# Performance work log

Hardware: AMD Instinct MI355X
Metric: run time of the kernel (lower is better)

Reference implementation:

```python
import jax, jax.numpy as jnp
import numpy as np

N = 50000      # nodes
E = 600000     # edges (before self loops)
F_IN = 128     # num_features
HID = 64       # num_hidden (per-head out channels of conv1)
HEADS = 8
NCLS = 16      # num_classes
NC = 16        # n_components (k_ricci feature dim)
NCP = 16       # n_components_p (e_poinc feature dim)


def _glorot(key, shape):
    lim = float(np.sqrt(6.0 / (shape[0] + shape[1])))
    return jax.random.uniform(key, shape, jnp.float32, -lim, lim)


def setup_inputs() -> dict:
    key = jax.random.key(0)
    ks = jax.random.split(key, 16)
    H1 = HEADS * HID  # 512
    return {
        "x": jax.random.normal(ks[0], (N, F_IN), jnp.float32),
        "edge_index": jax.random.randint(ks[1], (2, E), 0, N, jnp.int32),
        "alpha": jnp.ones((), jnp.float32),  # alpha_hp scalar
        "k_ricci": jax.random.normal(ks[2], (E + N, NC), jnp.float32),
        "e_poinc": jax.random.normal(ks[3], (N, NCP), jnp.float32),
        # conv1 params
        "W_src1": _glorot(ks[4], (F_IN, H1)),
        "h1_w1": _glorot(ks[5], (NC, HID)),
        "h1_w2": _glorot(ks[6], (HID, HID)),
        "h1_b2": jnp.zeros((HID,), jnp.float32),
        "p1_w1": _glorot(ks[7], (NCP, H1)),
        "p1_w2": _glorot(ks[8], (H1, H1)),
        "p1_b2": jnp.zeros((H1,), jnp.float32),
        "bias1": jnp.zeros((H1,), jnp.float32),
        # conv2 params (heads=1, concat=False)
        "W_src2": _glorot(ks[9], (H1, NCLS)),
        "h2_w1": _glorot(ks[10], (NC, NCLS)),
        "h2_w2": _glorot(ks[11], (NCLS, NCLS)),
        "h2_b2": jnp.zeros((NCLS,), jnp.float32),
        "p2_w1": _glorot(ks[12], (NCP, NCLS)),
        "p2_w2": _glorot(ks[13], (NCLS, NCLS)),
        "p2_b2": jnp.zeros((NCLS,), jnp.float32),
        "bias2": jnp.zeros((NCLS,), jnp.float32),
    }


def _segment_softmax(logits, seg, n):
    # PyG-style softmax over variable-sized segments, per channel.
    m = jax.ops.segment_max(logits, seg, num_segments=n)
    e = jnp.exp(logits - m[seg])
    s = jax.ops.segment_sum(e, seg, num_segments=n)
    return e / (s[seg] + 1e-16)


def _gat_layer(x, src, dst, k_ricci, e_poinc, alpha_hp,
               W_src, hw1, hw2, hb2, pw1, pw2, pb2, bias, H, C, concat):
    n = x.shape[0]
    xh = (x @ W_src).reshape(n, H, C)                                   # [N,H,C]
    # hmpnn MLP on per-edge Ricci features, then segment-softmax over SOURCE node
    edge_w = jax.nn.leaky_relu(k_ricci @ hw1, 0.2) @ hw2 + hb2          # [E',C]
    a = _segment_softmax(edge_w, src, n)                                # [E',C]
    msg = a[:, None, :] * xh[src]                                       # [E',H,C]
    agg = jax.ops.segment_sum(msg, dst, num_segments=n)                 # [N,H,C]
    out = agg.reshape(n, H * C) if concat else agg.mean(axis=1)
    out = out + bias
    # ham MLP on per-node Poincare features (+ extra leaky_relu, slope 0.01)
    p = jax.nn.leaky_relu(jax.nn.leaky_relu(e_poinc @ pw1, 0.2) @ pw2 + pb2, 0.01)
    return out + alpha_hp * p


def reference(x, edge_index, alpha, k_ricci, e_poinc,
              W_src1, h1_w1, h1_w2, h1_b2, p1_w1, p1_w2, p1_b2, bias1,
              W_src2, h2_w1, h2_w2, h2_b2, p2_w1, p2_w2, p2_b2, bias2):
    n = x.shape[0]
    loops = jnp.arange(n, dtype=edge_index.dtype)
    src = jnp.concatenate([edge_index[0], loops])   # add_self_loops
    dst = jnp.concatenate([edge_index[1], loops])
    h = _gat_layer(x, src, dst, k_ricci, e_poinc, alpha,
                   W_src1, h1_w1, h1_w2, h1_b2, p1_w1, p1_w2, p1_b2, bias1,
                   HEADS, HID, True)
    h = jax.nn.relu(h)
    o = _gat_layer(h, src, dst, k_ricci, e_poinc, alpha,
                   W_src2, h2_w1, h2_w2, h2_b2, p2_w1, p2_w2, p2_b2, bias2,
                   1, NCLS, False)
    return jax.nn.log_softmax(o, axis=1)
```

## Files before the change

kernel.cpp:

```cpp
#include <hip/hip_runtime.h>
#include <math.h>

#define N_NODES 50000
#define M_PAD   50048
#define N_EDGES 600000
#define E_TOT   650000
#define F_IN    128
#define HID     64
#define HEADS   8
#define H1      512
#define NCLS    16
#define NC      16
#define NCP     16
#define NBLK    ((N_NODES + 255) / 256)

typedef unsigned short u16;
typedef unsigned char  u8;
typedef __attribute__((ext_vector_type(8))) short short8;
typedef __attribute__((ext_vector_type(4))) float f32x4;
typedef __attribute__((ext_vector_type(2))) float f32x2;

__device__ __forceinline__ float bf2f(u16 h) {
    return __uint_as_float(((unsigned)h) << 16);
}
__device__ __forceinline__ u16 f2bf(float f) {
    unsigned u = __float_as_uint(f);
    u += 0x7fffu + ((u >> 16) & 1u);
    return (u16)(u >> 16);
}
__device__ __forceinline__ int edge_src(const int* __restrict__ ei, int e) {
    return (e < N_EDGES) ? ei[e] : (e - N_EDGES);
}
__device__ __forceinline__ int edge_dst(const int* __restrict__ ei, int e) {
    return (e < N_EDGES) ? ei[N_EDGES + e] : (e - N_EDGES);
}

__device__ __forceinline__ void gload16(const void* g, void* l) {
    __builtin_amdgcn_global_load_lds(
        (const __attribute__((address_space(1))) unsigned int*)g,
        (__attribute__((address_space(3))) unsigned int*)l, 16, 0, 0);
}

__global__ __launch_bounds__(256) void count_k(const int* __restrict__ ei,
                                               int* __restrict__ src_cnt, int* __restrict__ dst_cnt) {
    int e = blockIdx.x * 256 + threadIdx.x;
    if (e >= E_TOT) return;
    atomicAdd(&src_cnt[edge_src(ei, e)], 1);
    atomicAdd(&dst_cnt[edge_dst(ei, e)], 1);
}

__global__ __launch_bounds__(256) void scanA_k(const int* __restrict__ src_cnt,
                                               const int* __restrict__ dst_cnt,
                                               int* __restrict__ partials) {
    int pass = blockIdx.x >= NBLK;
    int b = blockIdx.x - pass * NBLK;
    const int* cnt = pass ? dst_cnt : src_cnt;
    int idx = b * 256 + threadIdx.x;
    int v = (idx < N_NODES) ? cnt[idx] : 0;
    __shared__ int red[4];
    #pragma unroll
    for (int off = 32; off; off >>= 1) v += __shfl_down(v, off, 64);
    if ((threadIdx.x & 63) == 0) red[threadIdx.x >> 6] = v;
    __syncthreads();
    if (threadIdx.x == 0) partials[blockIdx.x] = red[0] + red[1] + red[2] + red[3];
}

__global__ __launch_bounds__(512) void scanB_k(int* __restrict__ partials) {
    __shared__ int lds[512];
    int t = threadIdx.x;
    int seg = t >> 8, i = t & 255;
    int v = (i < NBLK) ? partials[seg * NBLK + i] : 0;
    lds[t] = v;
    __syncthreads();
    for (int d = 1; d < 256; d <<= 1) {
        int x = (i >= d) ? lds[seg * 256 + i - d] : 0;
        __syncthreads();
        lds[t] += x;
        __syncthreads();
    }
    if (i < NBLK) partials[seg * NBLK + i] = lds[t] - v;
}

__global__ __launch_bounds__(256) void scanC_k(const int* __restrict__ src_cnt,
                                               const int* __restrict__ dst_cnt,
                                               const int* __restrict__ partials,
                                               int* __restrict__ src_off, int* __restrict__ dst_off) {
    int pass = blockIdx.x >= NBLK;
    int b = blockIdx.x - pass * NBLK;
    const int* cnt = pass ? dst_cnt : src_cnt;
    int* off = pass ? dst_off : src_off;
    int base = partials[blockIdx.x];
    __shared__ int lds[256];
    int t = threadIdx.x;
    int idx = b * 256 + t;
    int v = (idx < N_NODES) ? cnt[idx] : 0;
    lds[t] = v;
    __syncthreads();
    for (int d = 1; d < 256; d <<= 1) {
        int x = (t >= d) ? lds[t - d] : 0;
        __syncthreads();
        lds[t] += x;
        __syncthreads();
    }
    if (idx < N_NODES) off[idx] = base + lds[t] - v;
    if (b == 0 && t == 0) off[N_NODES] = E_TOT;
}

__global__ __launch_bounds__(256) void fill_csr_k(const int* __restrict__ ei,
                                                  const int* __restrict__ src_off, const int* __restrict__ dst_off,
                                                  int* __restrict__ src_cur, int* __restrict__ dst_cur,
                                                  int* __restrict__ src_list, int* __restrict__ rkd,
                                                  int* __restrict__ dsrc) {
    int e = blockIdx.x * 256 + threadIdx.x;
    if (e >= E_TOT) return;
    int s = edge_src(ei, e), d = edge_dst(ei, e);
    int pd = atomicAdd(&dst_cur[d], 1);
    int rd = dst_off[d] + pd;
    rkd[e] = rd;
    dsrc[rd] = s;
    int ps = atomicAdd(&src_cur[s], 1);
    src_list[src_off[s] + ps] = rd;
}

__global__ __launch_bounds__(256) void conv_a_k(const float* __restrict__ A, u16* __restrict__ Ap,
                                                int M, int Mp, int K) {
    int i = blockIdx.x * 256 + threadIdx.x;
    int total = (K >> 3) * Mp;
    if (i >= total) return;
    int r = i % Mp;
    int kb = i / Mp;
    u16* o = Ap + (size_t)i * 8;
    u16 tmp[8];
    if (r < M) {
        const float* a = A + (size_t)r * K + kb * 8;
        #pragma unroll
        for (int j = 0; j < 8; ++j) tmp[j] = f2bf(a[j]);
    } else {
        #pragma unroll
        for (int j = 0; j < 8; ++j) tmp[j] = 0;
    }
    *(ushort4*)o = *(ushort4*)tmp;
    *(ushort4*)(o + 4) = *(ushort4*)(tmp + 4);
}

__global__ __launch_bounds__(256) void conv_b_k(const float* __restrict__ B, u16* __restrict__ Bp,
                                                int K, int N) {
    int i = blockIdx.x * 256 + threadIdx.x;
    int total = (K >> 3) * N;
    if (i >= total) return;
    int n = i % N;
    int kb = i / N;
    u16 tmp[8];
    #pragma unroll
    for (int j = 0; j < 8; ++j) tmp[j] = f2bf(B[(size_t)(kb * 8 + j) * N + n]);
    u16* o = Bp + (size_t)i * 8;
    *(ushort4*)o = *(ushort4*)tmp;
    *(ushort4*)(o + 4) = *(ushort4*)(tmp + 4);
}

__device__ __forceinline__ void wfrag_one(const float* W, u16* o, int i, int K, int N) {
    int j = i & 7, lane = (i >> 3) & 63, rest = i >> 9;
    int nt = rest % (N / 16), ks = rest / (N / 16);
    int lm = lane & 15, quad = lane >> 4;
    int k = ks * 32 + quad * 8 + j, n = nt * 16 + lm;
    o[i] = (k < K) ? f2bf(W[(size_t)k * N + n]) : (u16)0;
}
__global__ __launch_bounds__(256) void wfrag_all_k(
    const float* __restrict__ h1w1, const float* __restrict__ h1w2,
    const float* __restrict__ h2w1, const float* __restrict__ h2w2,
    u16* __restrict__ w1f, u16* __restrict__ w2f,
    u16* __restrict__ w3f, u16* __restrict__ w4f) {
    int i = blockIdx.x * 256 + threadIdx.x;
    if (i < 2048)      wfrag_one(h1w1, w1f, i, 16, 64);
    else if (i < 6144) wfrag_one(h1w2, w2f, i - 2048, 64, 64);
    else if (i < 6656) wfrag_one(h2w1, w3f, i - 6144, 16, 16);
    else if (i < 7168) wfrag_one(h2w2, w4f, i - 6656, 16, 16);
}

template<int EPI>
__global__ __launch_bounds__(256) void mfma_gemm_k(
    const u16* __restrict__ Ap, const u16* __restrict__ Bp, u16* __restrict__ C,
    int M, int Mp, int Nn, int K,
    const float* __restrict__ bias, const u16* __restrict__ extra,
    const float* __restrict__ bias2, const float* __restrict__ alpha_p)
{
    __shared__ __align__(16) u16 LB[4][4096];
    const int t = threadIdx.x;
    const int wave = t >> 6, lane = t & 63;
    const int wm = (wave >> 1) * 64, wn = (wave & 1) * 64;
    const int lm = lane & 15, quad = lane >> 4;

    const int nwg = (int)(gridDim.y << 2);
    const int bid = (int)(blockIdx.y * 4 + blockIdx.x);
    const int qq = nwg >> 3, rr8 = nwg & 7;
    const int xcd = bid & 7, idx = bid >> 3;
    const int wg = (xcd < rr8 ? xcd * (qq + 1) : rr8 * (qq + 1) + (xcd - rr8) * qq) + idx;
    const int bn = (wg & 3) * 128;
    const int bm = (wg >> 2) * 128;

    const char* Ab = (const char*)Ap;
    const char* Bb = (const char*)Bp;

    f32x4 acc[4][4] = {};
    const int NT = K >> 5;

    auto stage = [&](int buf, int ts) {
        const int kb0 = ts * 4;
        #pragma unroll
        for (int h = 0; h < 2; ++h) {
            const int ob = h * 4096 + wave * 1024;
            const int kb = kb0 + (ob >> 11);
            const int rem = (ob & 1024) + lane * 16;
            gload16(Ab + ((size_t)kb * Mp + bm) * 16 + rem, (char*)LB[buf] + ob);
            gload16(Bb + ((size_t)kb * Nn + bn) * 16 + rem, (char*)LB[2 + buf] + ob);
        }
    };
    auto compute = [&](int cb) {
        const u16* As = LB[cb];
        const u16* Bs = LB[2 + cb];
        short8 af[4], bfv[4];
        #pragma unroll
        for (int mi = 0; mi < 4; ++mi)
            af[mi] = *(const short8*)(As + quad * 1024 + (wm + mi * 16 + lm) * 8);
        #pragma unroll
        for (int nj = 0; nj < 4; ++nj)
            bfv[nj] = *(const short8*)(Bs + quad * 1024 + (wn + nj * 16 + lm) * 8);
        #pragma unroll
        for (int mi = 0; mi < 4; ++mi)
            #pragma unroll
            for (int nj = 0; nj < 4; ++nj)
                acc[mi][nj] = __builtin_amdgcn_mfma_f32_16x16x32_bf16(af[mi], bfv[nj], acc[mi][nj], 0, 0, 0);
    };

    stage(0, 0);
    __syncthreads();
    int cur = 0;
    for (int ts = 0; ts < NT - 1; ++ts) {
        stage(cur ^ 1, ts + 1);
        compute(cur);
        __syncthreads();
        cur ^= 1;
    }
    compute(cur);
    __syncthreads();

    float* Tf = (float*)LB;
    const int lrow = t & 63, chunk = t >> 6;
    const int col0 = chunk * 32;
    const float alpha = (EPI == 0) ? 0.f : *alpha_p;
    #pragma unroll
    for (int pass = 0; pass < 2; ++pass) {
        if ((wave >> 1) == pass) {
            #pragma unroll
            for (int mi = 0; mi < 4; ++mi)
                #pragma unroll
                for (int r4 = 0; r4 < 4; ++r4) {
                    const int lr = mi * 16 + quad * 4 + r4;
                    const int sw = (lr & 7) << 2;
                    #pragma unroll
                    for (int nj = 0; nj < 4; ++nj)
                        Tf[lr * 128 + ((wn + nj * 16 + lm) ^ sw)] = acc[mi][nj][r4];
                }
        }
        __syncthreads();
        const int rr = bm + pass * 64 + lrow;
        if (rr < M) {
            const int sw = (lrow & 7) << 2;
            float v[32];
            #pragma unroll
            for (int j4 = 0; j4 < 8; ++j4) {
                float4 f = *(const float4*)&Tf[lrow * 128 + ((col0 + j4 * 4) ^ sw)];
                v[j4 * 4] = f.x; v[j4 * 4 + 1] = f.y; v[j4 * 4 + 2] = f.z; v[j4 * 4 + 3] = f.w;
            }
            const int gc0 = bn + col0;
            u16 pk[32];
            if (EPI == 0) {
                #pragma unroll
                for (int j = 0; j < 32; ++j) pk[j] = f2bf(v[j]);
            } else {
                const u16* ex = extra + (size_t)rr * Nn + gc0;
                #pragma unroll
                for (int g = 0; g < 4; ++g) {
                    short8 e8 = *(const short8*)(ex + g * 8);
                    #pragma unroll
                    for (int j = 0; j < 8; ++j) {
                        const int cj = g * 8 + j;
                        float vv = v[cj] + bias[gc0 + cj];
                        vv = vv > 0.f ? vv : 0.01f * vv;
                        float o = bf2f((u16)e8[j]) + bias2[gc0 + cj] + alpha * vv;
                        o = fmaxf(o, 0.f);
                        pk[cj] = f2bf(o);
                    }
                }
            }
            #pragma unroll
            for (int g = 0; g < 4; ++g)
                *(short8*)(C + (size_t)rr * Nn + gc0 + g * 8) = *(const short8*)&pk[g * 8];
        }
        __syncthreads();
    }
}

__global__ __launch_bounds__(256) void gemm_t1_k(
    const float* __restrict__ ep, const float* __restrict__ W, u16* __restrict__ t1p)
{
    __shared__ float Bs[16][64];
    const int bm = blockIdx.y * 64, bn = blockIdx.x * 64;
    const int t = threadIdx.x;
    const int tx = t & 15, ty = t >> 4;
    *(float4*)&Bs[t >> 4][(t & 15) * 4] = *(const float4*)&W[(size_t)(t >> 4) * H1 + bn + (t & 15) * 4];
    __syncthreads();
    const int r0 = bm + ty * 4;
    const int c0 = bn + tx * 4;
    for (int i = 0; i < 4; ++i) {
        int r = r0 + i;
        if (r >= N_NODES) continue;
        float av[16];
        #pragma unroll
        for (int j4 = 0; j4 < 16; j4 += 4) {
            float4 v = *(const float4*)(ep + (size_t)r * NCP + j4);
            av[j4] = v.x; av[j4 + 1] = v.y; av[j4 + 2] = v.z; av[j4 + 3] = v.w;
        }
        u16 pk[4];
        #pragma unroll
        for (int q = 0; q < 4; ++q) {
            float s = 0.f;
            #pragma unroll
            for (int k = 0; k < 16; ++k) s = fmaf(av[k], Bs[k][tx * 4 + q], s);
            s = s > 0.f ? s : 0.2f * s;
            pk[q] = f2bf(s);
        }
        u16* o = t1p + ((size_t)(c0 >> 3) * M_PAD + r) * 8 + (c0 & 7);
        *(ushort4*)o = *(ushort4*)pk;
    }
}

__global__ __launch_bounds__(256) void gemm_n16_k(
    const u16* __restrict__ A, const float* __restrict__ B, float* __restrict__ C,
    int M, int K)
{
    __shared__ float As[16][64];
    __shared__ float Bs[64][16];
    const int row0 = blockIdx.x * 16;
    const int t = threadIdx.x;
    const int r = t >> 4, c = t & 15;
    const int ar = t >> 4, ak4 = (t & 15) * 4;
    const int bk = t >> 2, bc4 = (t & 3) * 4;
    float acc = 0.f;
    for (int k0 = 0; k0 < K; k0 += 64) {
        float4 av = make_float4(0.f, 0.f, 0.f, 0.f);
        if (row0 + ar < M) {
            ushort4 h4 = *(const ushort4*)(A + (size_t)(row0 + ar) * K + k0 + ak4);
            av = make_float4(bf2f(h4.x), bf2f(h4.y), bf2f(h4.z), bf2f(h4.w));
        }
        *(float4*)&As[ar][ak4] = av;
        *(float4*)&Bs[bk][bc4] = *(const float4*)(B + (size_t)(k0 + bk) * 16 + bc4);
        __syncthreads();
        #pragma unroll
        for (int kk = 0; kk < 64; ++kk)
            acc = fmaf(As[r][kk], Bs[kk][c], acc);
        __syncthreads();
    }
    if (row0 + r < M) C[(size_t)(row0 + r) * 16 + c] = acc;
}

#define TSTR 72
__global__ __launch_bounds__(256) void edge_mlps_k(
    const float* __restrict__ kr, const int* __restrict__ rkd,
    const u16* __restrict__ w1f, const u16* __restrict__ w2f, const float* __restrict__ b2a,
    const u16* __restrict__ w3f, const u16* __restrict__ w4f, const float* __restrict__ b2b,
    u16* __restrict__ ebd, u16* __restrict__ ebd2)
{
    __shared__ __align__(16) u16 T[4][16 * TSTR];
    const int t = threadIdx.x, wv = t >> 6, lane = t & 63;
    const int lm = lane & 15, quad = lane >> 4;
    const int tile = blockIdx.x * 4 + wv;
    const int e0 = tile * 16;
    if (e0 >= E_TOT) return;
    u16* Tw = T[wv];

    short8 W1[4], W2[2][4];
    #pragma unroll
    for (int nt = 0; nt < 4; ++nt) W1[nt] = *(const short8*)(w1f + ((size_t)nt * 64 + lane) * 8);
    #pragma unroll
    for (int ks = 0; ks < 2; ++ks)
        #pragma unroll
        for (int nt = 0; nt < 4; ++nt)
            W2[ks][nt] = *(const short8*)(w2f + (((size_t)ks * 4 + nt) * 64 + lane) * 8);
    short8 W3 = *(const short8*)(w3f + (size_t)lane * 8);
    short8 W4 = *(const short8*)(w4f + (size_t)lane * 8);
    float b2av[4];
    #pragma unroll
    for (int nt = 0; nt < 4; ++nt) b2av[nt] = b2a[nt * 16 + lm];
    float b2bv = b2b[lm];

    short8 af = {};
    if (quad < 2) {
        const float* kp = kr + (size_t)(e0 + lm) * NC + quad * 8;
        float4 v0 = *(const float4*)kp;
        float4 v1 = *(const float4*)(kp + 4);
        u16 tmp[8] = {f2bf(v0.x), f2bf(v0.y), f2bf(v0.z), f2bf(v0.w),
                      f2bf(v1.x), f2bf(v1.y), f2bf(v1.z), f2bf(v1.w)};
        af = *(const short8*)tmp;
    }

    f32x4 a1[4] = {};
    #pragma unroll
    for (int nt = 0; nt < 4; ++nt)
        a1[nt] = __builtin_amdgcn_mfma_f32_16x16x32_bf16(af, W1[nt], a1[nt], 0, 0, 0);
    #pragma unroll
    for (int nt = 0; nt < 4; ++nt)
        #pragma unroll
        for (int r = 0; r < 4; ++r) {
            float v = a1[nt][r];
            v = v > 0.f ? v : 0.2f * v;
            Tw[(quad * 4 + r) * TSTR + nt * 16 + lm] = f2bf(v);
        }
    __builtin_amdgcn_s_waitcnt(0);

    short8 a2[2];
    #pragma unroll
    for (int ks = 0; ks < 2; ++ks)
        a2[ks] = *(const short8*)&Tw[lm * TSTR + ks * 32 + quad * 8];
    f32x4 c2[4] = {};
    #pragma unroll
    for (int nt = 0; nt < 4; ++nt)
        #pragma unroll
        for (int ks = 0; ks < 2; ++ks)
            c2[nt] = __builtin_amdgcn_mfma_f32_16x16x32_bf16(a2[ks], W2[ks][nt], c2[nt], 0, 0, 0);
    #pragma unroll
    for (int nt = 0; nt < 4; ++nt)
        #pragma unroll
        for (int r = 0; r < 4; ++r)
            Tw[(quad * 4 + r) * TSTR + nt * 16 + lm] = f2bf(__expf(c2[nt][r] + b2av[nt]));
    __builtin_amdgcn_s_waitcnt(0);
    #pragma unroll
    for (int p = 0; p < 2; ++p) {
        int c = p * 64 + lane;
        int row = c >> 3, off = (c & 7) * 8;
        int rd = rkd[e0 + row];
        short8 v = *(const short8*)&Tw[row * TSTR + off];
        *(short8*)(ebd + (size_t)rd * HID + off) = v;
    }

    f32x4 b1 = __builtin_amdgcn_mfma_f32_16x16x32_bf16(af, W3, (f32x4){}, 0, 0, 0);
    __builtin_amdgcn_s_waitcnt(0);
    #pragma unroll
    for (int r = 0; r < 4; ++r) {
        float v = b1[r];
        v = v > 0.f ? v : 0.2f * v;
        Tw[(quad * 4 + r) * TSTR + lm] = f2bf(v);
    }
    __builtin_amdgcn_s_waitcnt(0);
    short8 a3 = *(const short8*)&Tw[lm * TSTR + quad * 8];
    f32x4 c3 = __builtin_amdgcn_mfma_f32_16x16x32_bf16(a3, W4, (f32x4){}, 0, 0, 0);
    #pragma unroll
    for (int r = 0; r < 4; ++r)
        Tw[(quad * 4 + r) * TSTR + lm] = f2bf(__expf(c3[r] + b2bv));
    __builtin_amdgcn_s_waitcnt(0);
    if (lane < 32) {
        int row = lane >> 1, off = (lane & 1) * 8;
        int rd = rkd[e0 + row];
        short8 v = *(const short8*)&Tw[row * TSTR + off];
        *(short8*)(ebd2 + (size_t)rd * NCLS + off) = v;
    }
}

__global__ __launch_bounds__(256) void s1inv_k(
    const u16* __restrict__ ebd, const int* __restrict__ src_off, const int* __restrict__ src_list,
    u16* __restrict__ xb)
{
    __shared__ float sinv[4][64];
    int gid = blockIdx.x * 256 + threadIdx.x;
    int wid = gid >> 6, lane = gid & 63, wv = threadIdx.x >> 6;
    if (wid >= N_NODES) return;
    int o0 = src_off[wid], o1 = src_off[wid + 1];
    float s0 = 0.f, s1 = 0.f, s2 = 0.f, s3 = 0.f;
    int i = o0;
    for (; i + 3 < o1; i += 4) {
        int l0 = src_list[i], l1 = src_list[i + 1], l2 = src_list[i + 2], l3 = src_list[i + 3];
        s0 += bf2f(ebd[(size_t)l0 * HID + lane]);
        s1 += bf2f(ebd[(size_t)l1 * HID + lane]);
        s2 += bf2f(ebd[(size_t)l2 * HID + lane]);
        s3 += bf2f(ebd[(size_t)l3 * HID + lane]);
    }
    for (; i < o1; ++i) {
        int sl = src_list[i];
        s0 += bf2f(ebd[(size_t)sl * HID + lane]);
    }
    sinv[wv][lane] = 1.f / (((s0 + s1) + (s2 + s3)) + 1e-16f);
    __builtin_amdgcn_s_waitcnt(0);

    const u16* xr = xb + (size_t)wid * H1 + lane * 8;
    short8 x8 = *(const short8*)xr;
    float y[8];
    #pragma unroll
    for (int j = 0; j < 8; ++j)
        y[j] = bf2f((u16)x8[j]) * sinv[wv][(lane * 8 + j) & 63];
    int p0 = 0, p1 = 0;
    p0 = __builtin_amdgcn_cvt_pk_fp8_f32(y[0], y[1], p0, false);
    p0 = __builtin_amdgcn_cvt_pk_fp8_f32(y[2], y[3], p0, true);
    p1 = __builtin_amdgcn_cvt_pk_fp8_f32(y[4], y[5], p1, false);
    p1 = __builtin_amdgcn_cvt_pk_fp8_f32(y[6], y[7], p1, true);
    uint2 pk; pk.x = (unsigned)p0; pk.y = (unsigned)p1;
    *(uint2*)((u8*)xb + (size_t)wid * (H1 * 2) + lane * 8) = pk;
}

__global__ __launch_bounds__(256) void msg1_k(
    const u16* __restrict__ ebd, const u8* __restrict__ xq,
    const int* __restrict__ dsrc, const int* __restrict__ dst_off,
    u16* __restrict__ aggb)
{
    int gid = blockIdx.x * 256 + threadIdx.x;
    int wid = gid >> 6, lane = gid & 63;
    if (wid >= N_NODES) return;
    int o0 = dst_off[wid], o1 = dst_off[wid + 1];
    const int a_off = (lane & 7) * 8;
    float acc[8] = {};
    int i = o0;
    for (; i + 3 < o1; i += 4) {
        int s0 = __builtin_nontemporal_load(dsrc + i);
        int s1 = __builtin_nontemporal_load(dsrc + i + 1);
        int s2 = __builtin_nontemporal_load(dsrc + i + 2);
        int s3 = __builtin_nontemporal_load(dsrc + i + 3);
        short8 a0 = __builtin_nontemporal_load((const short8*)(ebd + (size_t)i * HID + a_off));
        short8 a1 = __builtin_nontemporal_load((const short8*)(ebd + (size_t)(i + 1) * HID + a_off));
        short8 a2 = __builtin_nontemporal_load((const short8*)(ebd + (size_t)(i + 2) * HID + a_off));
        short8 a3 = __builtin_nontemporal_load((const short8*)(ebd + (size_t)(i + 3) * HID + a_off));
        uint2 q0 = *(const uint2*)(xq + (size_t)s0 * 1024 + lane * 8);
        uint2 q1 = *(const uint2*)(xq + (size_t)s1 * 1024 + lane * 8);
        uint2 q2 = *(const uint2*)(xq + (size_t)s2 * 1024 + lane * 8);
        uint2 q3 = *(const uint2*)(xq + (size_t)s3 * 1024 + lane * 8);
        const uint2 qs[4] = {q0, q1, q2, q3};
        const short8 as[4] = {a0, a1, a2, a3};
        #pragma unroll
        for (int u = 0; u < 4; ++u) {
            f32x2 d0 = __builtin_amdgcn_cvt_pk_f32_fp8((int)qs[u].x, false);
            f32x2 d1 = __builtin_amdgcn_cvt_pk_f32_fp8((int)qs[u].x, true);
            f32x2 d2 = __builtin_amdgcn_cvt_pk_f32_fp8((int)qs[u].y, false);
            f32x2 d3 = __builtin_amdgcn_cvt_pk_f32_fp8((int)qs[u].y, true);
            float xv[8] = {d0.x, d0.y, d1.x, d1.y, d2.x, d2.y, d3.x, d3.y};
            #pragma unroll
            for (int j = 0; j < 8; ++j)
                acc[j] = fmaf(bf2f((u16)as[u][j]), xv[j], acc[j]);
        }
    }
    for (; i < o1; ++i) {
        int s = __builtin_nontemporal_load(dsrc + i);
        short8 a8 = __builtin_nontemporal_load((const short8*)(ebd + (size_t)i * HID + a_off));
        uint2 q = *(const uint2*)(xq + (size_t)s * 1024 + lane * 8);
        f32x2 d0 = __builtin_amdgcn_cvt_pk_f32_fp8((int)q.x, false);
        f32x2 d1 = __builtin_amdgcn_cvt_pk_f32_fp8((int)q.x, true);
        f32x2 d2 = __builtin_amdgcn_cvt_pk_f32_fp8((int)q.y, false);
        f32x2 d3 = __builtin_amdgcn_cvt_pk_f32_fp8((int)q.y, true);
        float xv[8] = {d0.x, d0.y, d1.x, d1.y, d2.x, d2.y, d3.x, d3.y};
        #pragma unroll
        for (int j = 0; j < 8; ++j)
            acc[j] = fmaf(bf2f((u16)a8[j]), xv[j], acc[j]);
    }
    u16 pk[8];
    #pragma unroll
    for (int j = 0; j < 8; ++j) pk[j] = f2bf(acc[j]);
    __builtin_nontemporal_store(*(const short8*)pk, (short8*)(aggb + (size_t)wid * H1 + lane * 8));
}

__global__ __launch_bounds__(256) void s2sum_k(
    const u16* __restrict__ ebd2, const int* __restrict__ src_off, const int* __restrict__ src_list,
    float* __restrict__ inv2)
{
    int t = threadIdx.x;
    int g = blockIdx.x * 16 + (t >> 4), c = t & 15;
    if (g >= N_NODES) return;
    int o0 = src_off[g], o1 = src_off[g + 1];
    float sum = 0.f;
    for (int i = o0; i < o1; ++i) {
        int sl = src_list[i];
        sum += bf2f(ebd2[(size_t)sl * NCLS + c]);
    }
    inv2[(size_t)g * NCLS + c] = 1.f / (sum + 1e-16f);
}

__global__ __launch_bounds__(256) void msg2_k(
    const u16* __restrict__ ebd2, const float* __restrict__ inv2,
    const float* __restrict__ xh2, const int* __restrict__ dsrc,
    const int* __restrict__ dst_off, float* __restrict__ agg2)
{
    int t = threadIdx.x;
    int g = blockIdx.x * 16 + (t >> 4), c = t & 15;
    if (g >= N_NODES) return;
    int o0 = dst_off[g], o1 = dst_off[g + 1];
    float acc = 0.f;
    for (int i = o0; i < o1; ++i) {
        int s = dsrc[i];
        float a = bf2f(ebd2[(size_t)i * NCLS + c]) * inv2[(size_t)s * NCLS + c];
        acc = fmaf(a, xh2[(size_t)s * NCLS + c], acc);
    }
    agg2[(size_t)g * NCLS + c] = acc;
}

__global__ __launch_bounds__(256) void final_k(
    const float* __restrict__ agg2, const float* __restrict__ ep,
    const float* __restrict__ pw1, const float* __restrict__ pw2,
    const float* __restrict__ pb2, const float* __restrict__ bias,
    const float* __restrict__ alpha_p, float* __restrict__ out)
{
    __shared__ float s1w[256], s2w[256], sb[16], sbias[16];
    const int t = threadIdx.x;
    s1w[t] = pw1[t];
    s2w[t] = pw2[t];
    if (t < 16) { sb[t] = pb2[t]; sbias[t] = bias[t]; }
    __syncthreads();
    const int v = blockIdx.x * 256 + t;
    if (v >= N_NODES) return;
    float alpha = *alpha_p;
    float e_[16];
    #pragma unroll
    for (int j4 = 0; j4 < 16; j4 += 4) {
        float4 vv = *(const float4*)(ep + (size_t)v * 16 + j4);
        e_[j4] = vv.x; e_[j4 + 1] = vv.y; e_[j4 + 2] = vv.z; e_[j4 + 3] = vv.w;
    }
    float t2[16];
    #pragma unroll
    for (int c = 0; c < 16; ++c) {
        float s = 0.f;
        #pragma unroll
        for (int j = 0; j < 16; ++j) s = fmaf(e_[j], s1w[j * 16 + c], s);
        t2[c] = s > 0.f ? s : 0.2f * s;
    }
    float o[16];
    #pragma unroll
    for (int c4 = 0; c4 < 16; c4 += 4) {
        float4 ag = *(const float4*)(agg2 + (size_t)v * 16 + c4);
        float agv[4] = {ag.x, ag.y, ag.z, ag.w};
        #pragma unroll
        for (int q = 0; q < 4; ++q) {
            int c = c4 + q;
            float p = sb[c];
            #pragma unroll
            for (int j = 0; j < 16; ++j) p = fmaf(t2[j], s2w[j * 16 + c], p);
            p = p > 0.f ? p : 0.01f * p;
            o[c] = agv[q] + sbias[c] + alpha * p;
        }
    }
    float mx = o[0];
    #pragma unroll
    for (int c = 1; c < 16; ++c) mx = fmaxf(mx, o[c]);
    float se = 0.f;
    #pragma unroll
    for (int c = 0; c < 16; ++c) se += expf(o[c] - mx);
    float lse = mx + logf(se);
    #pragma unroll
    for (int c4 = 0; c4 < 16; c4 += 4)
        *(float4*)(out + (size_t)v * 16 + c4) =
            make_float4(o[c4] - lse, o[c4 + 1] - lse, o[c4 + 2] - lse, o[c4 + 3] - lse);
}

extern "C" void kernel_launch(void* const* d_in, const int* in_sizes, int n_in,
                              void* d_out, int out_size, void* d_ws, size_t ws_size,
                              hipStream_t stream) {
    const float* x    = (const float*)d_in[0];
    const int*   ei   = (const int*)d_in[1];
    const float* alpha= (const float*)d_in[2];
    const float* kr   = (const float*)d_in[3];
    const float* ep   = (const float*)d_in[4];
    const float* W1   = (const float*)d_in[5];
    const float* h1w1 = (const float*)d_in[6];
    const float* h1w2 = (const float*)d_in[7];
    const float* h1b2 = (const float*)d_in[8];
    const float* p1w1 = (const float*)d_in[9];
    const float* p1w2 = (const float*)d_in[10];
    const float* p1b2 = (const float*)d_in[11];
    const float* b1   = (const float*)d_in[12];
    const float* W2   = (const float*)d_in[13];
    const float* h2w1 = (const float*)d_in[14];
    const float* h2w2 = (const float*)d_in[15];
    const float* h2b2 = (const float*)d_in[16];
    const float* p2w1 = (const float*)d_in[17];
    const float* p2w2 = (const float*)d_in[18];
    const float* p2b2 = (const float*)d_in[19];
    const float* b2   = (const float*)d_in[20];
    float* out = (float*)d_out;

    char* p = (char*)d_ws;
    auto alloc = [&](size_t bytes) { char* r = p; p += (bytes + 255) & ~(size_t)255; return r; };

    char* r0    = alloc((size_t)64 * M_PAD * 16);
    u16*  xb    = (u16*)r0;
    u16*  t1p   = (u16*)r0;
    u16*  aggb  = (u16*)alloc((size_t)N_NODES * H1 * 2);
    char* ebr   = alloc((size_t)E_TOT * HID * 2);
    u16*  ebd   = (u16*)ebr;
    u16*  hb    = (u16*)ebr;
    u16*  ebd2  = (u16*)alloc((size_t)E_TOT * NCLS * 2);
    u16*  xp    = (u16*)alloc((size_t)16 * M_PAD * 16);
    u16*  W1p   = (u16*)alloc((size_t)16 * H1 * 16);
    u16*  p1w2p = (u16*)alloc((size_t)64 * H1 * 16);
    u16*  w1f   = (u16*)alloc(2048 * 2);
    u16*  w2f   = (u16*)alloc(4096 * 2);
    u16*  w3f   = (u16*)alloc(512 * 2);
    u16*  w4f   = (u16*)alloc(512 * 2);
    int* src_cnt  = (int*)alloc(N_NODES * 4);
    int* dst_cnt  = (int*)alloc(N_NODES * 4);
    int* src_cur  = (int*)alloc(N_NODES * 4);
    int* dst_cur  = (int*)alloc(N_NODES * 4);
    int* partials = (int*)alloc(2 * NBLK * 4);
    int* src_off  = (int*)alloc((N_NODES + 1) * 4);
    int* dst_off  = (int*)alloc((N_NODES + 1) * 4);
    int* src_list = (int*)alloc((size_t)E_TOT * 4);
    int* rkd      = (int*)alloc((size_t)E_TOT * 4);
    int* dsrc     = (int*)alloc((size_t)E_TOT * 4);
    float* xh2  = (float*)alloc((size_t)N_NODES * NCLS * 4);
    float* agg2 = (float*)alloc((size_t)N_NODES * NCLS * 4);
    float* inv2 = (float*)alloc((size_t)N_NODES * NCLS * 4);

    const dim3 blk(256);
    const int EB = (E_TOT + 255) / 256;
    const int WB = (N_NODES * 64 + 255) / 256;
    const int GB16 = (N_NODES + 15) / 16;
    const dim3 gmm(512 / 128, M_PAD / 128);
    const int MLPB = (E_TOT / 16 + 3) / 4;

    hipMemsetAsync(src_cnt, 0, (char*)partials - (char*)src_cnt, stream);
    count_k<<<EB, blk, 0, stream>>>(ei, src_cnt, dst_cnt);
    scanA_k<<<2 * NBLK, blk, 0, stream>>>(src_cnt, dst_cnt, partials);
    scanB_k<<<1, 512, 0, stream>>>(partials);
    scanC_k<<<2 * NBLK, blk, 0, stream>>>(src_cnt, dst_cnt, partials, src_off, dst_off);
    fill_csr_k<<<EB, blk, 0, stream>>>(ei, src_off, dst_off, src_cur, dst_cur, src_list, rkd, dsrc);
    conv_a_k<<<(16 * M_PAD + 255) / 256, blk, 0, stream>>>(x, xp, N_NODES, M_PAD, F_IN);
    conv_b_k<<<(16 * H1 + 255) / 256, blk, 0, stream>>>(W1, W1p, F_IN, H1);
    conv_b_k<<<(64 * H1 + 255) / 256, blk, 0, stream>>>(p1w2, p1w2p, H1, H1);
    wfrag_all_k<<<28, blk, 0, stream>>>(h1w1, h1w2, h2w1, h2w2, w1f, w2f, w3f, w4f);

    mfma_gemm_k<0><<<gmm, blk, 0, stream>>>(xp, W1p, xb, N_NODES, M_PAD, H1, F_IN,
                                            nullptr, nullptr, nullptr, nullptr);
    edge_mlps_k<<<MLPB, blk, 0, stream>>>(kr, rkd, w1f, w2f, h1b2, w3f, w4f, h2b2, ebd, ebd2);
    s1inv_k<<<WB, blk, 0, stream>>>(ebd, src_off, src_list, xb);
    msg1_k<<<WB, blk, 0, stream>>>(ebd, (const u8*)xb, dsrc, dst_off, aggb);
    gemm_t1_k<<<dim3(8, (N_NODES + 63) / 64), blk, 0, stream>>>(ep, p1w1, t1p);
    mfma_gemm_k<3><<<gmm, blk, 0, stream>>>(t1p, p1w2p, hb, N_NODES, M_PAD, H1, H1,
                                            p1b2, aggb, b1, alpha);

    gemm_n16_k<<<(N_NODES + 15) / 16, blk, 0, stream>>>(hb, W2, xh2, N_NODES, H1);
    s2sum_k<<<GB16, blk, 0, stream>>>(ebd2, src_off, src_list, inv2);
    msg2_k<<<GB16, blk, 0, stream>>>(ebd2, inv2, xh2, dsrc, dst_off, agg2);
    final_k<<<(N_NODES + 255) / 256, blk, 0, stream>>>(agg2, ep, p2w1, p2w2, p2b2, b2, alpha, out);
}
```

Before: 688.0 us.

## Load MFMA fragments directly from global into registers, dropping LDS staging

The bf16 MFMA GEMM no longer stages A/B tiles through LDS with global_load_lds and per-step barriers. Each wave now reads its pre-fragmented operands straight from global memory into registers, double-buffering two register sets across K steps. K becomes a template parameter so the loop trip count is known at compile time. The LDS is now used only for the epilogue transpose. This removes the barriers and LDS round trips, but both waves that share a row or column band now fetch it separately, so the kernel relies on cache hits and pays more global traffic and register pressure.

```diff
diff --git a/kernel.cpp b/kernel.cpp
--- a/kernel.cpp
+++ b/kernel.cpp
@@ -33,12 +33,6 @@
 }
 __device__ __forceinline__ int edge_dst(const int* __restrict__ ei, int e) {
     return (e < N_EDGES) ? ei[N_EDGES + e] : (e - N_EDGES);
-}
-
-__device__ __forceinline__ void gload16(const void* g, void* l) {
-    __builtin_amdgcn_global_load_lds(
-        (const __attribute__((address_space(1))) unsigned int*)g,
-        (__attribute__((address_space(3))) unsigned int*)l, 16, 0, 0);
 }
 
 __global__ __launch_bounds__(256) void count_k(const int* __restrict__ ei,
@@ -177,14 +171,14 @@
     else if (i < 7168) wfrag_one(h2w2, w4f, i - 6656, 16, 16);
 }
 
-template<int EPI>
+template<int EPI, int KK>
 __global__ __launch_bounds__(256) void mfma_gemm_k(
     const u16* __restrict__ Ap, const u16* __restrict__ Bp, u16* __restrict__ C,
-    int M, int Mp, int Nn, int K,
+    int M, int Mp, int Nn,
     const float* __restrict__ bias, const u16* __restrict__ extra,
     const float* __restrict__ bias2, const float* __restrict__ alpha_p)
 {
-    __shared__ __align__(16) u16 LB[4][4096];
+    __shared__ __align__(16) float Tf[64 * 128];
     const int t = threadIdx.x;
     const int wave = t >> 6, lane = t & 63;
     const int wm = (wave >> 1) * 64, wn = (wave & 1) * 64;
@@ -198,53 +192,46 @@
     const int bn = (wg & 3) * 128;
     const int bm = (wg >> 2) * 128;
 
-    const char* Ab = (const char*)Ap;
-    const char* Bb = (const char*)Bp;
+    size_t rbase[4], cbase[4];
+    #pragma unroll
+    for (int mi = 0; mi < 4; ++mi) rbase[mi] = (size_t)(bm + wm + mi * 16 + lm) * 8;
+    #pragma unroll
+    for (int nj = 0; nj < 4; ++nj) cbase[nj] = (size_t)(bn + wn + nj * 16 + lm) * 8;
+    const u16* Aq = Ap + (size_t)quad * Mp * 8;
+    const u16* Bq = Bp + (size_t)quad * Nn * 8;
 
     f32x4 acc[4][4] = {};
-    const int NT = K >> 5;
-
-    auto stage = [&](int buf, int ts) {
-        const int kb0 = ts * 4;
-        #pragma unroll
-        for (int h = 0; h < 2; ++h) {
-            const int ob = h * 4096 + wave * 1024;
-            const int kb = kb0 + (ob >> 11);
-            const int rem = (ob & 1024) + lane * 16;
-            gload16(Ab + ((size_t)kb * Mp + bm) * 16 + rem, (char*)LB[buf] + ob);
-            gload16(Bb + ((size_t)kb * Nn + bn) * 16 + rem, (char*)LB[2 + buf] + ob);
-        }
+    constexpr int NT = KK >> 5;
+
+    auto LOADF = [&](short8 (&af)[4], short8 (&bf)[4], int ts) {
+        const size_t ao = (size_t)ts * Mp * 32;
+        const size_t bo = (size_t)ts * Nn * 32;
+        #pragma unroll
+        for (int mi = 0; mi < 4; ++mi) af[mi] = *(const short8*)(Aq + ao + rbase[mi]);
+        #pragma unroll
+        for (int nj = 0; nj < 4; ++nj) bf[nj] = *(const short8*)(Bq + bo + cbase[nj]);
     };
-    auto compute = [&](int cb) {
-        const u16* As = LB[cb];
-        const u16* Bs = LB[2 + cb];
-        short8 af[4], bfv[4];
-        #pragma unroll
-        for (int mi = 0; mi < 4; ++mi)
-            af[mi] = *(const short8*)(As + quad * 1024 + (wm + mi * 16 + lm) * 8);
-        #pragma unroll
-        for (int nj = 0; nj < 4; ++nj)
-            bfv[nj] = *(const short8*)(Bs + quad * 1024 + (wn + nj * 16 + lm) * 8);
+    auto FMA = [&](short8 (&af)[4], short8 (&bf)[4]) {
         #pragma unroll
         for (int mi = 0; mi < 4; ++mi)
             #pragma unroll
             for (int nj = 0; nj < 4; ++nj)
-                acc[mi][nj] = __builtin_amdgcn_mfma_f32_16x16x32_bf16(af[mi], bfv[nj], acc[mi][nj], 0, 0, 0);
+                acc[mi][nj] = __builtin_amdgcn_mfma_f32_16x16x32_bf16(af[mi], bf[nj], acc[mi][nj], 0, 0, 0);
     };
 
-    stage(0, 0);
-    __syncthreads();
-    int cur = 0;
-    for (int ts = 0; ts < NT - 1; ++ts) {
-        stage(cur ^ 1, ts + 1);
-        compute(cur);
-        __syncthreads();
-        cur ^= 1;
-    }
-    compute(cur);
-    __syncthreads();
-
-    float* Tf = (float*)LB;
+    short8 aA[4], bA[4], aB[4], bB[4];
+    LOADF(aA, bA, 0);
+    #pragma unroll 1
+    for (int ts = 0; ts + 2 < NT; ts += 2) {
+        LOADF(aB, bB, ts + 1);
+        FMA(aA, bA);
+        LOADF(aA, bA, ts + 2);
+        FMA(aB, bB);
+    }
+    LOADF(aB, bB, NT - 1);
+    FMA(aA, bA);
+    FMA(aB, bB);
+
     const int lrow = t & 63, chunk = t >> 6;
     const int col0 = chunk * 32;
     const float alpha = (EPI == 0) ? 0.f : *alpha_p;
@@ -731,14 +718,14 @@
     conv_b_k<<<(64 * H1 + 255) / 256, blk, 0, stream>>>(p1w2, p1w2p, H1, H1);
     wfrag_all_k<<<28, blk, 0, stream>>>(h1w1, h1w2, h2w1, h2w2, w1f, w2f, w3f, w4f);
 
-    mfma_gemm_k<0><<<gmm, blk, 0, stream>>>(xp, W1p, xb, N_NODES, M_PAD, H1, F_IN,
-                                            nullptr, nullptr, nullptr, nullptr);
+    mfma_gemm_k<0, 128><<<gmm, blk, 0, stream>>>(xp, W1p, xb, N_NODES, M_PAD, H1,
+                                                 nullptr, nullptr, nullptr, nullptr);
     edge_mlps_k<<<MLPB, blk, 0, stream>>>(kr, rkd, w1f, w2f, h1b2, w3f, w4f, h2b2, ebd, ebd2);
     s1inv_k<<<WB, blk, 0, stream>>>(ebd, src_off, src_list, xb);
     msg1_k<<<WB, blk, 0, stream>>>(ebd, (const u8*)xb, dsrc, dst_off, aggb);
     gemm_t1_k<<<dim3(8, (N_NODES + 63) / 64), blk, 0, stream>>>(ep, p1w1, t1p);
-    mfma_gemm_k<3><<<gmm, blk, 0, stream>>>(t1p, p1w2p, hb, N_NODES, M_PAD, H1, H1,
-                                            p1b2, aggb, b1, alpha);
+    mfma_gemm_k<3, 512><<<gmm, blk, 0, stream>>>(t1p, p1w2p, hb, N_NODES, M_PAD, H1,
+                                                 p1b2, aggb, b1, alpha);
 
     gemm_n16_k<<<(N_NODES + 15) / 16, blk, 0, stream>>>(hb, W2, xh2, N_NODES, H1);
     s2sum_k<<<GB16, blk, 0, stream>>>(ebd2, src_off, src_list, inv2);
```

Measured after the change: 692.4 us. Within noise of the previous version (+0.6%).

## Split CSR fill into range-partitioned dst/src passes and gather edge inputs

Applied to the files above, without the earlier changes.

Replaces the single CSR-fill kernel with two passes. Each block handles one of eight node ranges over a slice of edges, so the atomics and scattered writes stay within a smaller address window. The src list is now built from the dst-sorted order, and the edge MLP gathers k_ricci rows by edge id and writes its outputs contiguously in dst-sorted order instead of scattering them. The cost is reading the edge list eight times per pass and adding an extra kernel launch in exchange for better write locality.

```diff
diff --git a/kernel.cpp b/kernel.cpp
--- a/kernel.cpp
+++ b/kernel.cpp
@@ -13,6 +13,9 @@
 #define NC      16
 #define NCP     16
 #define NBLK    ((N_NODES + 255) / 256)
+#define FRNG    (N_NODES / 8)
+#define FBPR    128
+#define FPER    ((E_TOT + FBPR - 1) / FBPR)
 
 typedef unsigned short u16;
 typedef unsigned char  u8;
@@ -106,20 +109,34 @@
     if (b == 0 && t == 0) off[N_NODES] = E_TOT;
 }
 
-__global__ __launch_bounds__(256) void fill_csr_k(const int* __restrict__ ei,
-                                                  const int* __restrict__ src_off, const int* __restrict__ dst_off,
-                                                  int* __restrict__ src_cur, int* __restrict__ dst_cur,
-                                                  int* __restrict__ src_list, int* __restrict__ rkd,
-                                                  int* __restrict__ dsrc) {
-    int e = blockIdx.x * 256 + threadIdx.x;
-    if (e >= E_TOT) return;
-    int s = edge_src(ei, e), d = edge_dst(ei, e);
-    int pd = atomicAdd(&dst_cur[d], 1);
-    int rd = dst_off[d] + pd;
-    rkd[e] = rd;
-    dsrc[rd] = s;
-    int ps = atomicAdd(&src_cur[s], 1);
-    src_list[src_off[s] + ps] = rd;
+__global__ __launch_bounds__(256) void fillD_k(const int* __restrict__ ei,
+                                               const int* __restrict__ dst_off, int* __restrict__ dst_cur,
+                                               int* __restrict__ deid, int* __restrict__ dsrc) {
+    const int range = blockIdx.x & 7, slice = blockIdx.x >> 3;
+    const int d0 = range * FRNG, d1 = d0 + FRNG;
+    const int e0 = slice * FPER;
+    const int e1 = (e0 + FPER < E_TOT) ? e0 + FPER : E_TOT;
+    for (int e = e0 + threadIdx.x; e < e1; e += 256) {
+        int d = edge_dst(ei, e);
+        if (d < d0 || d >= d1) continue;
+        int rd = dst_off[d] + atomicAdd(&dst_cur[d], 1);
+        deid[rd] = e;
+        dsrc[rd] = edge_src(ei, e);
+    }
+}
+
+__global__ __launch_bounds__(256) void fillS_k(const int* __restrict__ dsrc,
+                                               const int* __restrict__ src_off, int* __restrict__ src_cur,
+                                               int* __restrict__ src_list) {
+    const int range = blockIdx.x & 7, slice = blockIdx.x >> 3;
+    const int s0 = range * FRNG, s1 = s0 + FRNG;
+    const int r0 = slice * FPER;
+    const int r1 = (r0 + FPER < E_TOT) ? r0 + FPER : E_TOT;
+    for (int rd = r0 + threadIdx.x; rd < r1; rd += 256) {
+        int s = dsrc[rd];
+        if (s < s0 || s >= s1) continue;
+        src_list[src_off[s] + atomicAdd(&src_cur[s], 1)] = rd;
+    }
 }
 
 __global__ __launch_bounds__(256) void conv_a_k(const float* __restrict__ A, u16* __restrict__ Ap,
@@ -366,7 +383,7 @@
 
 #define TSTR 72
 __global__ __launch_bounds__(256) void edge_mlps_k(
-    const float* __restrict__ kr, const int* __restrict__ rkd,
+    const float* __restrict__ kr, const int* __restrict__ deid,
     const u16* __restrict__ w1f, const u16* __restrict__ w2f, const float* __restrict__ b2a,
     const u16* __restrict__ w3f, const u16* __restrict__ w4f, const float* __restrict__ b2b,
     u16* __restrict__ ebd, u16* __restrict__ ebd2)
@@ -375,8 +392,8 @@
     const int t = threadIdx.x, wv = t >> 6, lane = t & 63;
     const int lm = lane & 15, quad = lane >> 4;
     const int tile = blockIdx.x * 4 + wv;
-    const int e0 = tile * 16;
-    if (e0 >= E_TOT) return;
+    const int s0 = tile * 16;
+    if (s0 >= E_TOT) return;
     u16* Tw = T[wv];
 
     short8 W1[4], W2[2][4];
@@ -394,9 +411,10 @@
     for (int nt = 0; nt < 4; ++nt) b2av[nt] = b2a[nt * 16 + lm];
     float b2bv = b2b[lm];
 
+    const int e = deid[s0 + lm];
     short8 af = {};
     if (quad < 2) {
-        const float* kp = kr + (size_t)(e0 + lm) * NC + quad * 8;
+        const float* kp = kr + (size_t)e * NC + quad * 8;
         float4 v0 = *(const float4*)kp;
         float4 v1 = *(const float4*)(kp + 4);
         u16 tmp[8] = {f2bf(v0.x), f2bf(v0.y), f2bf(v0.z), f2bf(v0.w),
@@ -438,9 +456,8 @@
     for (int p = 0; p < 2; ++p) {
         int c = p * 64 + lane;
         int row = c >> 3, off = (c & 7) * 8;
-        int rd = rkd[e0 + row];
         short8 v = *(const short8*)&Tw[row * TSTR + off];
-        *(short8*)(ebd + (size_t)rd * HID + off) = v;
+        *(short8*)(ebd + (size_t)(s0 + row) * HID + off) = v;
     }
 
     f32x4 b1 = __builtin_amdgcn_mfma_f32_16x16x32_bf16(af, W3, (f32x4){}, 0, 0, 0);
@@ -460,9 +477,8 @@
     __builtin_amdgcn_s_waitcnt(0);
     if (lane < 32) {
         int row = lane >> 1, off = (lane & 1) * 8;
-        int rd = rkd[e0 + row];
         short8 v = *(const short8*)&Tw[row * TSTR + off];
-        *(short8*)(ebd2 + (size_t)rd * NCLS + off) = v;
+        *(short8*)(ebd2 + (size_t)(s0 + row) * NCLS + off) = v;
     }
 }
 
@@ -707,7 +723,7 @@
     int* src_off  = (int*)alloc((N_NODES + 1) * 4);
     int* dst_off  = (int*)alloc((N_NODES + 1) * 4);
     int* src_list = (int*)alloc((size_t)E_TOT * 4);
-    int* rkd      = (int*)alloc((size_t)E_TOT * 4);
+    int* deid     = (int*)alloc((size_t)E_TOT * 4);
     int* dsrc     = (int*)alloc((size_t)E_TOT * 4);
     float* xh2  = (float*)alloc((size_t)N_NODES * NCLS * 4);
     float* agg2 = (float*)alloc((size_t)N_NODES * NCLS * 4);
@@ -725,7 +741,8 @@
     scanA_k<<<2 * NBLK, blk, 0, stream>>>(src_cnt, dst_cnt, partials);
     scanB_k<<<1, 512, 0, stream>>>(partials);
     scanC_k<<<2 * NBLK, blk, 0, stream>>>(src_cnt, dst_cnt, partials, src_off, dst_off);
-    fill_csr_k<<<EB, blk, 0, stream>>>(ei, src_off, dst_off, src_cur, dst_cur, src_list, rkd, dsrc);
+    fillD_k<<<8 * FBPR, blk, 0, stream>>>(ei, dst_off, dst_cur, deid, dsrc);
+    fillS_k<<<8 * FBPR, blk, 0, stream>>>(dsrc, src_off, src_cur, src_list);
     conv_a_k<<<(16 * M_PAD + 255) / 256, blk, 0, stream>>>(x, xp, N_NODES, M_PAD, F_IN);
     conv_b_k<<<(16 * H1 + 255) / 256, blk, 0, stream>>>(W1, W1p, F_IN, H1);
     conv_b_k<<<(64 * H1 + 255) / 256, blk, 0, stream>>>(p1w2, p1w2p, H1, H1);
@@ -733,7 +750,7 @@
 
     mfma_gemm_k<0><<<gmm, blk, 0, stream>>>(xp, W1p, xb, N_NODES, M_PAD, H1, F_IN,
                                             nullptr, nullptr, nullptr, nullptr);
-    edge_mlps_k<<<MLPB, blk, 0, stream>>>(kr, rkd, w1f, w2f, h1b2, w3f, w4f, h2b2, ebd, ebd2);
+    edge_mlps_k<<<MLPB, blk, 0, stream>>>(kr, deid, w1f, w2f, h1b2, w3f, w4f, h2b2, ebd, ebd2);
     s1inv_k<<<WB, blk, 0, stream>>>(ebd, src_off, src_list, xb);
     msg1_k<<<WB, blk, 0, stream>>>(ebd, (const u8*)xb, dsrc, dst_off, aggb);
     gemm_t1_k<<<dim3(8, (N_NODES + 63) / 64), blk, 0, stream>>>(ep, p1w1, t1p);
```

Measured after the change: 670.3 us. 1.03x faster.
